# Kernel optimization log

Measured on AMD Instinct MI355X. Metric: run time of the kernel, lower is better.

Reference implementation:

```python
import jax, jax.numpy as jnp
import numpy as np

B, S, D, H = 1, 4096, 1024, 16
HD = D // H  # head_dim = 64


def setup_inputs() -> dict:
    key = jax.random.key(0)
    k1, k2, k3 = jax.random.split(key, 3)
    scale = 0.02
    return {
        "x": jax.random.normal(k1, (B, S, D), dtype=jnp.float32),
        "w_qkv": jax.random.normal(k2, (D, 3 * D), dtype=jnp.float32) * scale,
        "b_qkv": jnp.zeros((3 * D,), dtype=jnp.float32),
        "w_proj": jax.random.normal(k3, (D, D), dtype=jnp.float32) * scale,
        "b_proj": jnp.zeros((D,), dtype=jnp.float32),
    }


def reference(x, w_qkv, b_qkv, w_proj, b_proj):
    b, s, d = x.shape
    qkv = x @ w_qkv + b_qkv                      # [b, s, 3d]
    q, k, v = jnp.split(qkv, 3, axis=-1)
    # [b, h, s, hd]
    q = q.reshape(b, s, H, HD).transpose(0, 2, 1, 3)
    k = k.reshape(b, s, H, HD).transpose(0, 2, 1, 3)
    v = v.reshape(b, s, H, HD).transpose(0, 2, 1, 3)
    score = jnp.einsum("bhqd,bhkd->bhqk", q, k) / jnp.sqrt(jnp.float32(HD))
    causal = jnp.tril(jnp.ones((s, s), dtype=bool))
    score = jnp.where(causal, score, -jnp.inf)
    attn = jax.nn.softmax(score, axis=-1)        # dropout omitted (eval mode, p effectively 0)
    out = jnp.einsum("bhqk,bhkd->bhqd", attn, v)  # [b, h, s, hd]
    out = out.transpose(0, 2, 1, 3).reshape(b, s, d)
    return out @ w_proj + b_proj
```

## Files before the change

kernel.cpp:

```cpp
#include <hip/hip_runtime.h>
#include <hip/hip_bf16.h>
#include <math.h>

typedef __bf16 bf16;
typedef __bf16 bf16x8 __attribute__((ext_vector_type(8)));
typedef __bf16 bf16x4 __attribute__((ext_vector_type(4)));
typedef float f32x4 __attribute__((ext_vector_type(4)));

#define S_ 4096
#define D_ 1024
#define H_ 16
#define HD_ 64
#define N3_ 3072
#define NSPLIT 2

typedef const __attribute__((address_space(1))) void* gas1_t;
typedef __attribute__((address_space(3))) void* las3_t;
static __device__ __forceinline__ void g2l16(const void* g, void* l) {
  __builtin_amdgcn_global_load_lds((gas1_t)g, (las3_t)l, 16, 0, 0);
}

__global__ __launch_bounds__(256) void prep_kernel(const float* __restrict__ x,
                                                   bf16* __restrict__ xb,
                                                   const float* __restrict__ w_qkv,
                                                   bf16* __restrict__ wqkvT,
                                                   const float* __restrict__ w_proj,
                                                   bf16* __restrict__ wprojT) {
  __shared__ float t[32][33];
  const int b = blockIdx.x;
  if (b < 4096) {
    int i = (b * 256 + threadIdx.x) * 4;
    float4 v = *(const float4*)(x + i);
    bf16x4 o;
    o.x = (bf16)v.x; o.y = (bf16)v.y; o.z = (bf16)v.z; o.w = (bf16)v.w;
    *(bf16x4*)(xb + i) = o;
    return;
  }
  const float* in; bf16* outp; int ldin, bx, by;
  if (b < 7168) { int b2 = b - 4096; in = w_qkv;  outp = wqkvT;  ldin = N3_; bx = (b2 % 96) * 32; by = (b2 / 96) * 32; }
  else          { int b3 = b - 7168; in = w_proj; outp = wprojT; ldin = D_;  bx = (b3 % 32) * 32; by = (b3 / 32) * 32; }
  const int tx = threadIdx.x & 31, ty = threadIdx.x >> 5;
#pragma unroll
  for (int i = 0; i < 4; ++i)
    t[ty + i * 8][tx] = in[(size_t)(by + ty + i * 8) * ldin + bx + tx];
  __syncthreads();
#pragma unroll
  for (int i = 0; i < 4; ++i)
    outp[(size_t)(bx + ty + i * 8) * D_ + by + tx] = (bf16)t[tx][ty + i * 8];
}

template <int BN>
__global__ __launch_bounds__(256) void gemm_bt(const bf16* __restrict__ A,
                                               const bf16* __restrict__ Bt,
                                               const float* __restrict__ bias,
                                               bf16* __restrict__ outb,
                                               float* __restrict__ outf,
                                               bf16* __restrict__ vTout,
                                               int M, int N, int K,
                                               int qlim, float qscale) {
  constexpr int NT = BN / 32;
  __shared__ bf16 sA[128 * 32];
  __shared__ bf16 sB[BN * 32];
  const int tid = threadIdx.x;
  const int wave = tid >> 6, lane = tid & 63;
  const int col = lane & 15, quad = lane >> 4;
  const int wm = (wave & 1) * 64, wn = (wave >> 1) * (BN / 2);
  const long bm = (long)blockIdx.x * 128, bn = (long)blockIdx.y * BN;
  const int srow = tid >> 2;
  const int soff = (tid & 3) * 8;

  f32x4 acc[4][NT] = {};

  for (int kb = 0; kb < K; kb += 32) {
    __syncthreads();
    g2l16(A + (bm + srow) * (long)K + kb + soff,      &sA[tid * 8]);
    g2l16(A + (bm + 64 + srow) * (long)K + kb + soff, &sA[2048 + tid * 8]);
#pragma unroll
    for (int i = 0; i < BN / 64; ++i)
      g2l16(Bt + (bn + i * 64 + srow) * (long)K + kb + soff, &sB[i * 2048 + tid * 8]);
    __syncthreads();

    bf16x8 af[4], bfr[NT];
#pragma unroll
    for (int t = 0; t < 4; ++t)
      af[t] = *(const bf16x8*)(&sA[(wm + t * 16 + col) * 32 + quad * 8]);
#pragma unroll
    for (int t = 0; t < NT; ++t)
      bfr[t] = *(const bf16x8*)(&sB[(wn + t * 16 + col) * 32 + quad * 8]);
#pragma unroll
    for (int mt = 0; mt < 4; ++mt)
#pragma unroll
      for (int nt = 0; nt < NT; ++nt)
        acc[mt][nt] = __builtin_amdgcn_mfma_f32_16x16x32_bf16(af[mt], bfr[nt], acc[mt][nt], 0, 0, 0);
  }

#pragma unroll
  for (int mt = 0; mt < 4; ++mt) {
#pragma unroll
    for (int nt = 0; nt < NT; ++nt) {
      long gn = bn + wn + nt * 16 + col;
      float bv = bias ? bias[gn] : 0.f;
      if (vTout && gn >= 2 * D_) {
        bf16x4 vv;
        long gm0 = bm + wm + mt * 16 + quad * 4;
#pragma unroll
        for (int i = 0; i < 4; ++i) vv[i] = (bf16)(acc[mt][nt][i] + bv);
        *(bf16x4*)(&vTout[(gn - 2 * D_) * (long)S_ + gm0]) = vv;
      } else {
        float sc = (gn < qlim) ? qscale : 1.0f;
#pragma unroll
        for (int i = 0; i < 4; ++i) {
          long gm = bm + wm + mt * 16 + quad * 4 + i;
          float v = (acc[mt][nt][i] + bv) * sc;
          if (outf) outf[gm * N + gn] = v;
          else      outb[gm * N + gn] = (bf16)v;
        }
      }
    }
  }
}

__global__ __launch_bounds__(512, 2) void gemm256_qkv(const bf16* __restrict__ A,
                                                      const bf16* __restrict__ Bt,
                                                      const float* __restrict__ bias,
                                                      bf16* __restrict__ outb,
                                                      bf16* __restrict__ vTout,
                                                      float qscale) {
  __shared__ bf16 smem[65536];
  const int K = D_;
  const int NTK = K / 64;
  const int tid = threadIdx.x;
  const int lane = tid & 63, wv = tid >> 6;
  const int col = lane & 15, quad = lane >> 4;
  const int wr = wv >> 2, wc = wv & 3;
  const long bm = (long)blockIdx.x * 256, bn = (long)blockIdx.y * 256;

  int srowA[2][2], srowB[2][2];
  int schA[2][2], schB[2][2];
#pragma unroll
  for (int q = 0; q < 2; ++q) {
    int slot = q * 512 + tid;
    int rl = slot >> 3, ch = slot & 7;
#pragma unroll
    for (int h = 0; h < 2; ++h) {
      int rowA = (rl & 63) | (h << 6) | ((rl >> 6) << 7);
      srowA[h][q] = rowA; schA[h][q] = ch ^ (rowA & 7);
      int rowB = (rl & 31) | (h << 5) | ((rl >> 5) << 6);
      srowB[h][q] = rowB; schB[h][q] = ch ^ (rowB & 7);
    }
  }
  const int dstoff = tid * 8;

  const int ck[2] = { ((0 * 4 + quad) ^ (col & 7)) * 8, ((1 * 4 + quad) ^ (col & 7)) * 8 };

#define STAGE_A(h, T, buf)                                                        \
  {                                                                               \
    const int kbs = (T) * 64;                                                     \
    bf16* lb = smem + (buf) * 32768 + (h) * 8192;                                 \
    g2l16(A + (bm + srowA[h][0]) * (long)K + kbs + schA[h][0] * 8, lb + dstoff);  \
    g2l16(A + (bm + srowA[h][1]) * (long)K + kbs + schA[h][1] * 8, lb + 4096 + dstoff); \
  }
#define STAGE_B(h, T, buf)                                                        \
  {                                                                               \
    const int kbs = (T) * 64;                                                     \
    bf16* lb = smem + (buf) * 32768 + 16384 + (h) * 8192;                         \
    g2l16(Bt + (bn + srowB[h][0]) * (long)K + kbs + schB[h][0] * 8, lb + dstoff); \
    g2l16(Bt + (bn + srowB[h][1]) * (long)K + kbs + schB[h][1] * 8, lb + 4096 + dstoff); \
  }

  f32x4 acc[8][4] = {};

  STAGE_A(0, 0, 0);
  STAGE_A(1, 0, 0);
  STAGE_B(0, 0, 0);
  STAGE_A(0, 1, 1);
  STAGE_B(1, 0, 0);

  for (int G = 0; G < NTK; ++G) {
    const int cur = G & 1;
    const bf16* bufc = smem + cur * 32768;
    const bool last = (G == NTK - 1);

    bf16x8 afr[4][2], bfr[2][2][2];

    if (last) asm volatile("s_waitcnt vmcnt(2)" ::: "memory");
    else      asm volatile("s_waitcnt vmcnt(4)" ::: "memory");
    __builtin_amdgcn_s_barrier();
    __builtin_amdgcn_sched_barrier(0);
#pragma unroll
    for (int mt = 0; mt < 4; ++mt) {
      const bf16* rp = bufc + (wr * 64 + mt * 16 + col) * 64;
      afr[mt][0] = *(const bf16x8*)(rp + ck[0]);
      afr[mt][1] = *(const bf16x8*)(rp + ck[1]);
    }
#pragma unroll
    for (int nt = 0; nt < 2; ++nt) {
      const bf16* rp = bufc + 16384 + (wc * 32 + nt * 16 + col) * 64;
      bfr[0][nt][0] = *(const bf16x8*)(rp + ck[0]);
      bfr[0][nt][1] = *(const bf16x8*)(rp + ck[1]);
    }
    if (G + 1 < NTK) STAGE_A(1, G + 1, cur ^ 1);
    asm volatile("s_waitcnt lgkmcnt(0)" ::: "memory");
    __builtin_amdgcn_sched_barrier(0);
    __builtin_amdgcn_s_setprio(1);
#pragma unroll
    for (int mt = 0; mt < 4; ++mt)
#pragma unroll
      for (int nt = 0; nt < 2; ++nt) {
        acc[mt][nt] = __builtin_amdgcn_mfma_f32_16x16x32_bf16(afr[mt][0], bfr[0][nt][0], acc[mt][nt], 0, 0, 0);
        acc[mt][nt] = __builtin_amdgcn_mfma_f32_16x16x32_bf16(afr[mt][1], bfr[0][nt][1], acc[mt][nt], 0, 0, 0);
      }
    __builtin_amdgcn_s_setprio(0);

    if (last) asm volatile("s_waitcnt vmcnt(0)" ::: "memory");
    else      asm volatile("s_waitcnt vmcnt(2)" ::: "memory");
    __builtin_amdgcn_s_barrier();
    __builtin_amdgcn_sched_barrier(0);
#pragma unroll
    for (int nt = 0; nt < 2; ++nt) {
      const bf16* rp = bufc + 16384 + 8192 + (wc * 32 + nt * 16 + col) * 64;
      bfr[1][nt][0] = *(const bf16x8*)(rp + ck[0]);
      bfr[1][nt][1] = *(const bf16x8*)(rp + ck[1]);
    }
    if (G + 1 < NTK) STAGE_B(0, G + 1, cur ^ 1);
    asm volatile("s_waitcnt lgkmcnt(0)" ::: "memory");
    __builtin_amdgcn_sched_barrier(0);
    __builtin_amdgcn_s_setprio(1);
#pragma unroll
    for (int mt = 0; mt < 4; ++mt)
#pragma unroll
      for (int nt = 0; nt < 2; ++nt) {
        acc[mt][2 + nt] = __builtin_amdgcn_mfma_f32_16x16x32_bf16(afr[mt][0], bfr[1][nt][0], acc[mt][2 + nt], 0, 0, 0);
        acc[mt][2 + nt] = __builtin_amdgcn_mfma_f32_16x16x32_bf16(afr[mt][1], bfr[1][nt][1], acc[mt][2 + nt], 0, 0, 0);
      }
    __builtin_amdgcn_s_setprio(0);

    __builtin_amdgcn_s_barrier();
    __builtin_amdgcn_sched_barrier(0);
#pragma unroll
    for (int mt = 0; mt < 4; ++mt) {
      const bf16* rp = bufc + 8192 + (wr * 64 + mt * 16 + col) * 64;
      afr[mt][0] = *(const bf16x8*)(rp + ck[0]);
      afr[mt][1] = *(const bf16x8*)(rp + ck[1]);
    }
    if (G + 2 < NTK) STAGE_A(0, G + 2, cur);
    asm volatile("s_waitcnt lgkmcnt(0)" ::: "memory");
    __builtin_amdgcn_sched_barrier(0);
    __builtin_amdgcn_s_setprio(1);
#pragma unroll
    for (int mt = 0; mt < 4; ++mt)
#pragma unroll
      for (int nt = 0; nt < 2; ++nt) {
        acc[4 + mt][2 + nt] = __builtin_amdgcn_mfma_f32_16x16x32_bf16(afr[mt][0], bfr[1][nt][0], acc[4 + mt][2 + nt], 0, 0, 0);
        acc[4 + mt][2 + nt] = __builtin_amdgcn_mfma_f32_16x16x32_bf16(afr[mt][1], bfr[1][nt][1], acc[4 + mt][2 + nt], 0, 0, 0);
      }
    __builtin_amdgcn_s_setprio(0);

    __builtin_amdgcn_s_barrier();
    __builtin_amdgcn_sched_barrier(0);
    if (G + 1 < NTK) STAGE_B(1, G + 1, cur ^ 1);
    __builtin_amdgcn_s_setprio(1);
#pragma unroll
    for (int mt = 0; mt < 4; ++mt)
#pragma unroll
      for (int nt = 0; nt < 2; ++nt) {
        acc[4 + mt][nt] = __builtin_amdgcn_mfma_f32_16x16x32_bf16(afr[mt][0], bfr[0][nt][0], acc[4 + mt][nt], 0, 0, 0);
        acc[4 + mt][nt] = __builtin_amdgcn_mfma_f32_16x16x32_bf16(afr[mt][1], bfr[0][nt][1], acc[4 + mt][nt], 0, 0, 0);
      }
    __builtin_amdgcn_s_setprio(0);
  }

  const bool isV = (blockIdx.y >= 8);
  const bool isQ = (blockIdx.y < 4);
#pragma unroll
  for (int mh = 0; mh < 2; ++mh)
#pragma unroll
    for (int mt = 0; mt < 4; ++mt)
#pragma unroll
      for (int nh = 0; nh < 2; ++nh)
#pragma unroll
        for (int nt = 0; nt < 2; ++nt) {
          long gn = bn + wc * 64 + nh * 32 + nt * 16 + col;
          float bv = bias[gn];
          long gm0 = bm + wr * 128 + mh * 64 + mt * 16 + quad * 4;
          f32x4 a = acc[mh * 4 + mt][nh * 2 + nt];
          if (isV) {
            bf16x4 vv;
#pragma unroll
            for (int i = 0; i < 4; ++i) vv[i] = (bf16)(a[i] + bv);
            *(bf16x4*)(&vTout[(gn - 2 * D_) * (long)S_ + gm0]) = vv;
          } else {
            float sc = isQ ? qscale : 1.0f;
#pragma unroll
            for (int i = 0; i < 4; ++i)
              outb[(gm0 + i) * (long)N3_ + gn] = (bf16)((a[i] + bv) * sc);
          }
        }
#undef STAGE_A
#undef STAGE_B
}

__device__ __forceinline__ int swz_g(int row) {
  return (row & 3) | ((((row >> 2) ^ (row >> 3)) & 1) << 2);
}

__global__ __launch_bounds__(256) void attn_kernel(const bf16* __restrict__ qkv,
                                                   const bf16* __restrict__ vT,
                                                   bf16* __restrict__ Opart,
                                                   float* __restrict__ lws) {
  __shared__ bf16 sK[4][64 * 64];
  __shared__ bf16 sV[4][64 * 64];
  const int hh = blockIdx.x;
  const int qb = (int)(gridDim.y - 1 - blockIdx.y);
  const int sp = blockIdx.z;
  const int tid = threadIdx.x;
  const int wave = tid >> 6, lane = tid & 63;
  const int col = lane & 15, quad = lane >> 4;
  const int qbase = qb * 128 + wave * 32;

  const bf16* qp0 = qkv + (size_t)(qbase + col) * N3_ + hh * HD_;
  bf16x8 aq[2][2];
  aq[0][0] = *(const bf16x8*)(qp0 + quad * 8);
  aq[0][1] = *(const bf16x8*)(qp0 + 32 + quad * 8);
  aq[1][0] = *(const bf16x8*)(qp0 + 16 * N3_ + quad * 8);
  aq[1][1] = *(const bf16x8*)(qp0 + 16 * N3_ + 32 + quad * 8);

  bf16x8 ones;
#pragma unroll
  for (int j = 0; j < 8; ++j) ones[j] = (bf16)1.0f;

  f32x4 acc[2][4] = {};
  f32x4 acc_l[2] = {};

  const bf16* kgbase = qkv + D_ + hh * HD_;
  const bf16* vgbase = vT + (size_t)hh * HD_ * S_;
  const int krow = (col >> 2) * 8 + (col & 3);
  const int niter = 2 * (qb + 1);
  const int len = niter / NSPLIT;
  const int it0 = sp * len;
  const int it1 = it0 + len;

  const int srow = tid >> 2;
  const int sc0 = (tid & 3) * 2;
  const int gs = swz_g(srow);
  const int soff0 = srow * 64 + ((sc0 ^ gs) * 8);
  const int soff1 = srow * 64 + (((sc0 + 1) ^ gs) * 8);

  {
    const bf16* kg = kgbase + (size_t)(it0 * 64 + srow) * N3_ + sc0 * 8;
    const bf16* vg = vgbase + (size_t)srow * S_ + it0 * 64 + sc0 * 8;
    *(int4*)(&sK[0][soff0]) = *(const int4*)kg;
    *(int4*)(&sK[0][soff1]) = *(const int4*)(kg + 8);
    *(int4*)(&sV[0][soff0]) = *(const int4*)vg;
    *(int4*)(&sV[0][soff1]) = *(const int4*)(vg + 8);
    if (it0 + 1 < it1) {
      const bf16* kg1 = kg + (size_t)64 * N3_;
      const bf16* vg1 = vg + 64;
      *(int4*)(&sK[1][soff0]) = *(const int4*)kg1;
      *(int4*)(&sK[1][soff1]) = *(const int4*)(kg1 + 8);
      *(int4*)(&sV[1][soff0]) = *(const int4*)vg1;
      *(int4*)(&sV[1][soff1]) = *(const int4*)(vg1 + 8);
    }
  }
  __syncthreads();

#define CHUNK_BODY(KB, BI)                                                        \
  if ((KB) < qbase + 32) {                                                        \
    const bool act0 = (KB) < qbase + 16;                                          \
    const bf16* kc = &sK[BI][0];                                                  \
    const bf16* vc = &sV[BI][0];                                                  \
    f32x4 st[2][4];                                                               \
    _Pragma("unroll")                                                             \
    for (int t = 0; t < 4; ++t) {                                                 \
      int row = (t >> 1) * 32 + (t & 1) * 4 + krow;                               \
      int pc = quad ^ swz_g(row);                                                 \
      bf16x8 kf0 = *(const bf16x8*)(kc + row * 64 + pc * 8);                      \
      bf16x8 kf1 = *(const bf16x8*)(kc + row * 64 + (pc ^ 4) * 8);                \
      if (act0) {                                                                 \
        f32x4 z = {};                                                             \
        z = __builtin_amdgcn_mfma_f32_16x16x32_bf16(kf0, aq[0][0], z, 0, 0, 0);   \
        st[0][t] = __builtin_amdgcn_mfma_f32_16x16x32_bf16(kf1, aq[0][1], z, 0, 0, 0); \
      }                                                                           \
      f32x4 z = {};                                                               \
      z = __builtin_amdgcn_mfma_f32_16x16x32_bf16(kf0, aq[1][0], z, 0, 0, 0);     \
      st[1][t] = __builtin_amdgcn_mfma_f32_16x16x32_bf16(kf1, aq[1][1], z, 0, 0, 0); \
    }                                                                             \
    bf16x8 pfrag[2][2];                                                           \
    _Pragma("unroll")                                                             \
    for (int s2 = 0; s2 < 2; ++s2) {                                              \
      if (s2 == 0 && !act0) continue;                                             \
      const int rowbase = qbase + 16 * s2;                                        \
      float p[4][4];                                                              \
      if ((KB) + 63 <= rowbase) {                                                 \
        _Pragma("unroll")                                                         \
        for (int t = 0; t < 4; ++t)                                               \
          _Pragma("unroll")                                                       \
          for (int r = 0; r < 4; ++r)                                             \
            p[t][r] = __builtin_amdgcn_exp2f(st[s2][t][r]);                       \
      } else {                                                                    \
        _Pragma("unroll")                                                         \
        for (int t = 0; t < 4; ++t)                                               \
          _Pragma("unroll")                                                       \
          for (int r = 0; r < 4; ++r) {                                           \
            int key = (KB) + (t >> 1) * 32 + quad * 8 + (t & 1) * 4 + r;          \
            p[t][r] = (key > rowbase + col) ? 0.f                                 \
                                            : __builtin_amdgcn_exp2f(st[s2][t][r]); \
          }                                                                       \
      }                                                                           \
      _Pragma("unroll")                                                           \
      for (int c = 0; c < 2; ++c)                                                 \
        _Pragma("unroll")                                                         \
        for (int j2 = 0; j2 < 4; ++j2) {                                          \
          pfrag[s2][c][j2]     = (bf16)p[2 * c][j2];                              \
          pfrag[s2][c][j2 + 4] = (bf16)p[2 * c + 1][j2];                          \
        }                                                                         \
    }                                                                             \
    _Pragma("unroll")                                                             \
    for (int c = 0; c < 2; ++c) {                                                 \
      _Pragma("unroll")                                                           \
      for (int n = 0; n < 4; ++n) {                                               \
        int row = n * 16 + col;                                                   \
        int pc = (4 * c + quad) ^ swz_g(row);                                     \
        bf16x8 vf = *(const bf16x8*)(vc + row * 64 + pc * 8);                     \
        if (act0)                                                                 \
          acc[0][n] = __builtin_amdgcn_mfma_f32_16x16x32_bf16(pfrag[0][c], vf, acc[0][n], 0, 0, 0); \
        acc[1][n] = __builtin_amdgcn_mfma_f32_16x16x32_bf16(pfrag[1][c], vf, acc[1][n], 0, 0, 0);   \
      }                                                                           \
      if (act0)                                                                   \
        acc_l[0] = __builtin_amdgcn_mfma_f32_16x16x32_bf16(pfrag[0][c], ones, acc_l[0], 0, 0, 0);   \
      acc_l[1] = __builtin_amdgcn_mfma_f32_16x16x32_bf16(pfrag[1][c], ones, acc_l[1], 0, 0, 0);     \
    }                                                                             \
  }

  for (int j0 = it0; j0 < it1; j0 += 2) {
    const int bb = (((j0 - it0) >> 1) & 1) * 2;
    const bool hasB = (j0 + 1 < it1);
    const bool pfA = (j0 + 2 < it1);
    const bool pfB = (j0 + 3 < it1);

    int4 nk00, nk01, nv00, nv01, nk10, nk11, nv10, nv11;
    if (pfA) {
      const bf16* kg = kgbase + (size_t)((j0 + 2) * 64 + srow) * N3_ + sc0 * 8;
      const bf16* vg = vgbase + (size_t)srow * S_ + (j0 + 2) * 64 + sc0 * 8;
      nk00 = *(const int4*)kg; nk01 = *(const int4*)(kg + 8);
      nv00 = *(const int4*)vg; nv01 = *(const int4*)(vg + 8);
    }
    if (pfB) {
      const bf16* kg = kgbase + (size_t)((j0 + 3) * 64 + srow) * N3_ + sc0 * 8;
      const bf16* vg = vgbase + (size_t)srow * S_ + (j0 + 3) * 64 + sc0 * 8;
      nk10 = *(const int4*)kg; nk11 = *(const int4*)(kg + 8);
      nv10 = *(const int4*)vg; nv11 = *(const int4*)(vg + 8);
    }

    {
      const int kb0 = j0 * 64;
      CHUNK_BODY(kb0, bb);
    }
    if (hasB) {
      const int kb1 = (j0 + 1) * 64;
      CHUNK_BODY(kb1, bb + 1);
    }

    if (pfA) {
      bf16* kn = &sK[bb ^ 2][0];
      bf16* vn = &sV[bb ^ 2][0];
      *(int4*)(kn + soff0) = nk00; *(int4*)(kn + soff1) = nk01;
      *(int4*)(vn + soff0) = nv00; *(int4*)(vn + soff1) = nv01;
    }
    if (pfB) {
      bf16* kn = &sK[(bb ^ 2) + 1][0];
      bf16* vn = &sV[(bb ^ 2) + 1][0];
      *(int4*)(kn + soff0) = nk10; *(int4*)(kn + soff1) = nk11;
      *(int4*)(vn + soff0) = nv10; *(int4*)(vn + soff1) = nv11;
    }
    __syncthreads();
  }
#undef CHUNK_BODY

  bf16* Op = Opart + (size_t)sp * S_ * D_;
#pragma unroll
  for (int s2 = 0; s2 < 2; ++s2) {
    const int rowbase = qbase + 16 * s2;
    if (col == 0) {
#pragma unroll
      for (int r = 0; r < 4; ++r)
        lws[((size_t)sp * H_ + hh) * S_ + rowbase + quad * 4 + r] = acc_l[s2][r];
    }
#pragma unroll
    for (int n = 0; n < 4; ++n)
#pragma unroll
      for (int r = 0; r < 4; ++r)
        Op[(size_t)(rowbase + quad * 4 + r) * D_ + hh * HD_ + n * 16 + col] =
            (bf16)acc[s2][n][r];
  }
}

__global__ __launch_bounds__(256) void attn_combine(const bf16* __restrict__ Opart,
                                                    const float* __restrict__ lws,
                                                    bf16* __restrict__ outb) {
  int e = (blockIdx.x * 256 + threadIdx.x) * 8;
  int s = e >> 10;
  int h = (e & (D_ - 1)) >> 6;
  float l = 0.f;
#pragma unroll
  for (int sp = 0; sp < NSPLIT; ++sp) l += lws[((size_t)sp * H_ + h) * S_ + s];
  float inv = 1.0f / l;
  float o[8] = {};
#pragma unroll
  for (int sp = 0; sp < NSPLIT; ++sp) {
    bf16x8 a = *(const bf16x8*)(Opart + (size_t)sp * S_ * D_ + e);
#pragma unroll
    for (int j = 0; j < 8; ++j) o[j] += (float)a[j];
  }
  bf16x8 r;
#pragma unroll
  for (int j = 0; j < 8; ++j) r[j] = (bf16)(o[j] * inv);
  *(bf16x8*)(outb + e) = r;
}

extern "C" void kernel_launch(void* const* d_in, const int* in_sizes, int n_in,
                              void* d_out, int out_size, void* d_ws, size_t ws_size,
                              hipStream_t stream) {
  const float* x      = (const float*)d_in[0];
  const float* w_qkv  = (const float*)d_in[1];
  const float* b_qkv  = (const float*)d_in[2];
  const float* w_proj = (const float*)d_in[3];
  const float* b_proj = (const float*)d_in[4];
  float* out = (float*)d_out;

  bf16* xb     = (bf16*)d_ws;
  bf16* wqkvT  = xb + (size_t)S_ * D_;
  bf16* wprojT = wqkvT + (size_t)N3_ * D_;
  bf16* qkv    = wprojT + (size_t)D_ * D_;
  bf16* vT     = qkv + (size_t)S_ * N3_;
  bf16* Opart  = vT + (size_t)D_ * S_;
  float* lws   = (float*)(Opart + (size_t)NSPLIT * S_ * D_);
  bf16* attn   = xb;

  const float QSCALE = 0.125f * 1.44269504088896f;

  prep_kernel<<<dim3(8192), 256, 0, stream>>>(x, xb, w_qkv, wqkvT, w_proj, wprojT);
  gemm256_qkv<<<dim3(S_ / 256, N3_ / 256), 512, 0, stream>>>(
      xb, wqkvT, b_qkv, qkv, vT, QSCALE);
  attn_kernel<<<dim3(H_, S_ / 128, NSPLIT), 256, 0, stream>>>(qkv, vT, Opart, lws);
  attn_combine<<<dim3((S_ * D_) / 2048), 256, 0, stream>>>(Opart, lws, attn);
  gemm_bt<64><<<dim3(S_ / 128, D_ / 64), 256, 0, stream>>>(
      attn, wprojT, b_proj, nullptr, out, nullptr, S_, D_, D_, 0, 1.0f);
}
```

Measured before the change: 195.3 us.

## Replace projection GEMM with double-buffered swizzled 128x128 pipelined kernel

Replaces the simple output-projection GEMM (128x64 tiles, K-step 32, two barriers per step with no overlap) with a 128x128-tile kernel. It uses K-step 64, XOR-swizzled LDS layout, double buffering with async global-to-LDS loads, and an interleaved four-phase schedule. Each phase loads half-tiles while MFMAs run, using explicit waitcnt, s_setprio and sched_barrier. The aim is to hide global load latency, reduce LDS bank conflicts and raise arithmetic intensity, at the cost of fewer blocks (256) and more complex hand-tuned synchronisation.

```diff
diff --git a/kernel.cpp b/kernel.cpp
--- a/kernel.cpp
+++ b/kernel.cpp
@@ -47,77 +47,6 @@
 #pragma unroll
   for (int i = 0; i < 4; ++i)
     outp[(size_t)(bx + ty + i * 8) * D_ + by + tx] = (bf16)t[tx][ty + i * 8];
-}
-
-template <int BN>
-__global__ __launch_bounds__(256) void gemm_bt(const bf16* __restrict__ A,
-                                               const bf16* __restrict__ Bt,
-                                               const float* __restrict__ bias,
-                                               bf16* __restrict__ outb,
-                                               float* __restrict__ outf,
-                                               bf16* __restrict__ vTout,
-                                               int M, int N, int K,
-                                               int qlim, float qscale) {
-  constexpr int NT = BN / 32;
-  __shared__ bf16 sA[128 * 32];
-  __shared__ bf16 sB[BN * 32];
-  const int tid = threadIdx.x;
-  const int wave = tid >> 6, lane = tid & 63;
-  const int col = lane & 15, quad = lane >> 4;
-  const int wm = (wave & 1) * 64, wn = (wave >> 1) * (BN / 2);
-  const long bm = (long)blockIdx.x * 128, bn = (long)blockIdx.y * BN;
-  const int srow = tid >> 2;
-  const int soff = (tid & 3) * 8;
-
-  f32x4 acc[4][NT] = {};
-
-  for (int kb = 0; kb < K; kb += 32) {
-    __syncthreads();
-    g2l16(A + (bm + srow) * (long)K + kb + soff,      &sA[tid * 8]);
-    g2l16(A + (bm + 64 + srow) * (long)K + kb + soff, &sA[2048 + tid * 8]);
-#pragma unroll
-    for (int i = 0; i < BN / 64; ++i)
-      g2l16(Bt + (bn + i * 64 + srow) * (long)K + kb + soff, &sB[i * 2048 + tid * 8]);
-    __syncthreads();
-
-    bf16x8 af[4], bfr[NT];
-#pragma unroll
-    for (int t = 0; t < 4; ++t)
-      af[t] = *(const bf16x8*)(&sA[(wm + t * 16 + col) * 32 + quad * 8]);
-#pragma unroll
-    for (int t = 0; t < NT; ++t)
-      bfr[t] = *(const bf16x8*)(&sB[(wn + t * 16 + col) * 32 + quad * 8]);
-#pragma unroll
-    for (int mt = 0; mt < 4; ++mt)
-#pragma unroll
-      for (int nt = 0; nt < NT; ++nt)
-        acc[mt][nt] = __builtin_amdgcn_mfma_f32_16x16x32_bf16(af[mt], bfr[nt], acc[mt][nt], 0, 0, 0);
-  }
-
-#pragma unroll
-  for (int mt = 0; mt < 4; ++mt) {
-#pragma unroll
-    for (int nt = 0; nt < NT; ++nt) {
-      long gn = bn + wn + nt * 16 + col;
-      float bv = bias ? bias[gn] : 0.f;
-      if (vTout && gn >= 2 * D_) {
-        bf16x4 vv;
-        long gm0 = bm + wm + mt * 16 + quad * 4;
-#pragma unroll
-        for (int i = 0; i < 4; ++i) vv[i] = (bf16)(acc[mt][nt][i] + bv);
-        *(bf16x4*)(&vTout[(gn - 2 * D_) * (long)S_ + gm0]) = vv;
-      } else {
-        float sc = (gn < qlim) ? qscale : 1.0f;
-#pragma unroll
-        for (int i = 0; i < 4; ++i) {
-          long gm = bm + wm + mt * 16 + quad * 4 + i;
-          float v = (acc[mt][nt][i] + bv) * sc;
-          if (outf) outf[gm * N + gn] = v;
-          else      outb[gm * N + gn] = (bf16)v;
-        }
-      }
-    }
-  }
 }
 
 __global__ __launch_bounds__(512, 2) void gemm256_qkv(const bf16* __restrict__ A,
@@ -518,6 +447,171 @@
   *(bf16x8*)(outb + e) = r;
 }
 
+__global__ __launch_bounds__(256, 2) void proj8_gemm(const bf16* __restrict__ A,
+                                                     const bf16* __restrict__ Bt,
+                                                     const float* __restrict__ bias,
+                                                     float* __restrict__ outf) {
+  __shared__ bf16 smem[32768];
+  const int K = D_;
+  const int NTK = K / 64;
+  const int tid = threadIdx.x;
+  const int lane = tid & 63, wv = tid >> 6;
+  const int col = lane & 15, quad = lane >> 4;
+  const int wr = wv >> 1, wc = wv & 1;
+  const long bm = (long)blockIdx.x * 128, bn = (long)blockIdx.y * 128;
+
+  int srow[2][2], sch[2][2];
+#pragma unroll
+  for (int q = 0; q < 2; ++q) {
+    int slot = q * 256 + tid;
+    int rl = slot >> 3, ch = slot & 7;
+#pragma unroll
+    for (int h = 0; h < 2; ++h) {
+      int row = (rl & 31) | (h << 5) | ((rl >> 5) << 6);
+      srow[h][q] = row; sch[h][q] = ch ^ (row & 7);
+    }
+  }
+  const int dstoff = tid * 8;
+
+  const int ck[2] = { ((0 * 4 + quad) ^ (col & 7)) * 8, ((1 * 4 + quad) ^ (col & 7)) * 8 };
+
+#define STAGE_PA(h, T, buf)                                                      \
+  {                                                                              \
+    const int kbs = (T) * 64;                                                    \
+    bf16* lb = smem + (buf) * 16384 + (h) * 4096;                                \
+    g2l16(A + (bm + srow[h][0]) * (long)K + kbs + sch[h][0] * 8, lb + dstoff);   \
+    g2l16(A + (bm + srow[h][1]) * (long)K + kbs + sch[h][1] * 8, lb + 2048 + dstoff); \
+  }
+#define STAGE_PB(h, T, buf)                                                      \
+  {                                                                              \
+    const int kbs = (T) * 64;                                                    \
+    bf16* lb = smem + (buf) * 16384 + 8192 + (h) * 4096;                         \
+    g2l16(Bt + (bn + srow[h][0]) * (long)K + kbs + sch[h][0] * 8, lb + dstoff);  \
+    g2l16(Bt + (bn + srow[h][1]) * (long)K + kbs + sch[h][1] * 8, lb + 2048 + dstoff); \
+  }
+
+  f32x4 acc[4][4] = {};
+
+  STAGE_PA(0, 0, 0);
+  STAGE_PA(1, 0, 0);
+  STAGE_PB(0, 0, 0);
+  STAGE_PA(0, 1, 1);
+  STAGE_PB(1, 0, 0);
+
+  for (int G = 0; G < NTK; ++G) {
+    const int cur = G & 1;
+    const bf16* bufc = smem + cur * 16384;
+    const bool last = (G == NTK - 1);
+
+    bf16x8 afr[2][2], bfr[2][2][2];
+
+    if (last) asm volatile("s_waitcnt vmcnt(2)" ::: "memory");
+    else      asm volatile("s_waitcnt vmcnt(4)" ::: "memory");
+    __builtin_amdgcn_s_barrier();
+    __builtin_amdgcn_sched_barrier(0);
+#pragma unroll
+    for (int mt = 0; mt < 2; ++mt) {
+      const bf16* rp = bufc + (wr * 32 + mt * 16 + col) * 64;
+      afr[mt][0] = *(const bf16x8*)(rp + ck[0]);
+      afr[mt][1] = *(const bf16x8*)(rp + ck[1]);
+    }
+#pragma unroll
+    for (int nt = 0; nt < 2; ++nt) {
+      const bf16* rp = bufc + 8192 + (wc * 32 + nt * 16 + col) * 64;
+      bfr[0][nt][0] = *(const bf16x8*)(rp + ck[0]);
+      bfr[0][nt][1] = *(const bf16x8*)(rp + ck[1]);
+    }
+    if (G + 1 < NTK) STAGE_PA(1, G + 1, cur ^ 1);
+    asm volatile("s_waitcnt lgkmcnt(0)" ::: "memory");
+    __builtin_amdgcn_sched_barrier(0);
+    __builtin_amdgcn_s_setprio(1);
+#pragma unroll
+    for (int mt = 0; mt < 2; ++mt)
+#pragma unroll
+      for (int nt = 0; nt < 2; ++nt) {
+        acc[mt][nt] = __builtin_amdgcn_mfma_f32_16x16x32_bf16(afr[mt][0], bfr[0][nt][0], acc[mt][nt], 0, 0, 0);
+        acc[mt][nt] = __builtin_amdgcn_mfma_f32_16x16x32_bf16(afr[mt][1], bfr[0][nt][1], acc[mt][nt], 0, 0, 0);
+      }
+    __builtin_amdgcn_s_setprio(0);
+
+    if (last) asm volatile("s_waitcnt vmcnt(0)" ::: "memory");
+    else      asm volatile("s_waitcnt vmcnt(2)" ::: "memory");
+    __builtin_amdgcn_s_barrier();
+    __builtin_amdgcn_sched_barrier(0);
+#pragma unroll
+    for (int nt = 0; nt < 2; ++nt) {
+      const bf16* rp = bufc + 8192 + 4096 + (wc * 32 + nt * 16 + col) * 64;
+      bfr[1][nt][0] = *(const bf16x8*)(rp + ck[0]);
+      bfr[1][nt][1] = *(const bf16x8*)(rp + ck[1]);
+    }
+    if (G + 1 < NTK) STAGE_PB(0, G + 1, cur ^ 1);
+    asm volatile("s_waitcnt lgkmcnt(0)" ::: "memory");
+    __builtin_amdgcn_sched_barrier(0);
+    __builtin_amdgcn_s_setprio(1);
+#pragma unroll
+    for (int mt = 0; mt < 2; ++mt)
+#pragma unroll
+      for (int nt = 0; nt < 2; ++nt) {
+        acc[mt][2 + nt] = __builtin_amdgcn_mfma_f32_16x16x32_bf16(afr[mt][0], bfr[1][nt][0], acc[mt][2 + nt], 0, 0, 0);
+        acc[mt][2 + nt] = __builtin_amdgcn_mfma_f32_16x16x32_bf16(afr[mt][1], bfr[1][nt][1], acc[mt][2 + nt], 0, 0, 0);
+      }
+    __builtin_amdgcn_s_setprio(0);
+
+    __builtin_amdgcn_s_barrier();
+    __builtin_amdgcn_sched_barrier(0);
+#pragma unroll
+    for (int mt = 0; mt < 2; ++mt) {
+      const bf16* rp = bufc + 4096 + (wr * 32 + mt * 16 + col) * 64;
+      afr[mt][0] = *(const bf16x8*)(rp + ck[0]);
+      afr[mt][1] = *(const bf16x8*)(rp + ck[1]);
+    }
+    if (G + 2 < NTK) STAGE_PA(0, G + 2, cur);
+    asm volatile("s_waitcnt lgkmcnt(0)" ::: "memory");
+    __builtin_amdgcn_sched_barrier(0);
+    __builtin_amdgcn_s_setprio(1);
+#pragma unroll
+    for (int mt = 0; mt < 2; ++mt)
+#pragma unroll
+      for (int nt = 0; nt < 2; ++nt) {
+        acc[2 + mt][2 + nt] = __builtin_amdgcn_mfma_f32_16x16x32_bf16(afr[mt][0], bfr[1][nt][0], acc[2 + mt][2 + nt], 0, 0, 0);
+        acc[2 + mt][2 + nt] = __builtin_amdgcn_mfma_f32_16x16x32_bf16(afr[mt][1], bfr[1][nt][1], acc[2 + mt][2 + nt], 0, 0, 0);
+      }
+    __builtin_amdgcn_s_setprio(0);
+
+    __builtin_amdgcn_s_barrier();
+    __builtin_amdgcn_sched_barrier(0);
+    if (G + 1 < NTK) STAGE_PB(1, G + 1, cur ^ 1);
+    __builtin_amdgcn_s_setprio(1);
+#pragma unroll
+    for (int mt = 0; mt < 2; ++mt)
+#pragma unroll
+      for (int nt = 0; nt < 2; ++nt) {
+        acc[2 + mt][nt] = __builtin_amdgcn_mfma_f32_16x16x32_bf16(afr[mt][0], bfr[0][nt][0], acc[2 + mt][nt], 0, 0, 0);
+        acc[2 + mt][nt] = __builtin_amdgcn_mfma_f32_16x16x32_bf16(afr[mt][1], bfr[0][nt][1], acc[2 + mt][nt], 0, 0, 0);
+      }
+    __builtin_amdgcn_s_setprio(0);
+  }
+
+#pragma unroll
+  for (int mh = 0; mh < 2; ++mh)
+#pragma unroll
+    for (int mt = 0; mt < 2; ++mt)
+#pragma unroll
+      for (int nh = 0; nh < 2; ++nh)
+#pragma unroll
+        for (int nt = 0; nt < 2; ++nt) {
+          long gn = bn + wc * 64 + nh * 32 + nt * 16 + col;
+          float bv = bias[gn];
+          long gm0 = bm + wr * 64 + mh * 32 + mt * 16 + quad * 4;
+          f32x4 a = acc[mh * 2 + mt][nh * 2 + nt];
+#pragma unroll
+          for (int i = 0; i < 4; ++i)
+            outf[(gm0 + i) * (long)D_ + gn] = a[i] + bv;
+        }
+#undef STAGE_PA
+#undef STAGE_PB
+}
+
 extern "C" void kernel_launch(void* const* d_in, const int* in_sizes, int n_in,
                               void* d_out, int out_size, void* d_ws, size_t ws_size,
                               hipStream_t stream) {
@@ -544,6 +638,6 @@
       xb, wqkvT, b_qkv, qkv, vT, QSCALE);
   attn_kernel<<<dim3(H_, S_ / 128, NSPLIT), 256, 0, stream>>>(qkv, vT, Opart, lws);
   attn_combine<<<dim3((S_ * D_) / 2048), 256, 0, stream>>>(Opart, lws, attn);
-  gemm_bt<64><<<dim3(S_ / 128, D_ / 64), 256, 0, stream>>>(
-      attn, wprojT, b_proj, nullptr, out, nullptr, S_, D_, D_, 0, 1.0f);
-}
+  proj8_gemm<<<dim3(S_ / 128, D_ / 128), 256, 0, stream>>>(
+      attn, wprojT, b_proj, out);
+}
```

New measurement: 190.8 us. -2.3%, faster.
